# Performance work log

Hardware: AMD Instinct MI355X
Metric: run time of the kernel (lower is better)

## Reference

```python
import jax, jax.numpy as jnp
import numpy as np

IN_CAPS, IN_SIZE = 1152, 8
OUT_CAPS, OUT_SIZE = 10, 16
NUM_ITERS = 3


def squash(s, axis=-1, eps=1e-8):
    sq = jnp.sum(s * s, axis=axis, keepdims=True)
    norm = jnp.sqrt(sq + eps)
    return (sq / (1.0 + sq)) * (s / norm)


def setup_inputs() -> dict:
    key = jax.random.key(0)
    kx, kw = jax.random.split(key)
    x = jax.random.normal(kx, (512, IN_CAPS, IN_SIZE), dtype=jnp.float32)
    W = jax.random.normal(kw, (IN_CAPS, OUT_CAPS, OUT_SIZE, IN_SIZE), dtype=jnp.float32)
    return {"x": x, "W": W}


def reference(x, W):
    # u_hat[b,i,o,p] = sum_q W[i,o,p,q] x[b,i,q]   -> [B, I, O, P]
    u_hat = jnp.einsum("iopq,biq->biop", W, x)
    b_ij = jnp.zeros((IN_CAPS, OUT_CAPS), dtype=u_hat.dtype)
    v_j = None
    for _ in range(NUM_ITERS):
        # legacy F.softmax on [1,I,O,1] with no dim -> softmax over dim=1 (in_capsules)
        c_ij = jax.nn.softmax(b_ij, axis=0)                      # [I, O]
        s_j = jnp.einsum("io,biop->bop", c_ij, u_hat)            # [B, O, P]
        v_j = squash(s_j, axis=-1)                               # [B, O, P]
        # agreement, averaged over batch
        u_vj1 = jnp.einsum("biop,bop->io", u_hat, v_j) / x.shape[0]
        b_ij = b_ij + u_vj1
    return v_j  # [B, 10, 16]
```

## Files before the change

kernel.cpp:

```cpp
#include <hip/hip_runtime.h>
#include <hip/hip_bf16.h>

#define B 512
#define IC 1152
#define QD 8
#define OD 10
#define PD 16
#define KD (IC * QD)
#define NKB (KD / 32)
#define NCS 72
#define KSTEPS (NKB / NCS)
#define NCB 4
#define SOP (B * OD * PD)
#define IO (IC * OD)

typedef short bf16x8 __attribute__((ext_vector_type(8)));
typedef float f32x4 __attribute__((ext_vector_type(4)));

__device__ __forceinline__ short f2bf(float f) {
  union { float f; unsigned u; } x;
  x.f = f;
  unsigned r = x.u + 0x7FFFu + ((x.u >> 16) & 1u);
  return (short)(r >> 16);
}

__global__ __launch_bounds__(256) void routebuild_kernel(const float* __restrict__ W,
                                                         const float* __restrict__ u_part,
                                                         float* __restrict__ bijA,
                                                         short* __restrict__ Bs,
                                                         int mode) {
  __shared__ float bl[IO];
  __shared__ float wred[4][OD];
  __shared__ float mx[OD], inv[OD];
  const int tid = threadIdx.x;
  const int wave = tid >> 6, lane = tid & 63;

  if (mode != 0) {
    float lmax[OD];
#pragma unroll
    for (int o = 0; o < OD; ++o) lmax[o] = -1e30f;
    for (int i = tid; i < IC; i += 256) {
      float acc[OD];
      if (mode == 2) {
#pragma unroll
        for (int o = 0; o < OD; ++o) acc[o] = bijA[i * OD + o];
      } else {
#pragma unroll
        for (int o = 0; o < OD; ++o) acc[o] = 0.f;
      }
      for (int bc = 0; bc < NCB; ++bc) {
        const float* up = u_part + (size_t)bc * IO + i * OD;
        const float4 u0 = *(const float4*)up;
        const float4 u1 = *(const float4*)(up + 4);
        const float2 u2 = *(const float2*)(up + 8);
        acc[0] += u0.x; acc[1] += u0.y; acc[2] += u0.z; acc[3] += u0.w;
        acc[4] += u1.x; acc[5] += u1.y; acc[6] += u1.z; acc[7] += u1.w;
        acc[8] += u2.x; acc[9] += u2.y;
      }
#pragma unroll
      for (int o = 0; o < OD; ++o) {
        bl[i * OD + o] = acc[o];
        lmax[o] = fmaxf(lmax[o], acc[o]);
        if (mode == 1 && blockIdx.x == 0) bijA[i * OD + o] = acc[o];
      }
    }
#pragma unroll
    for (int o = 0; o < OD; ++o) {
      float m = lmax[o];
#pragma unroll
      for (int s = 1; s < 64; s <<= 1) m = fmaxf(m, __shfl_xor(m, s));
      if (lane == 0) wred[wave][o] = m;
    }
    __syncthreads();
    if (tid < OD)
      mx[tid] = fmaxf(fmaxf(wred[0][tid], wred[1][tid]),
                      fmaxf(wred[2][tid], wred[3][tid]));
    __syncthreads();
    float lsum[OD];
#pragma unroll
    for (int o = 0; o < OD; ++o) lsum[o] = 0.f;
    for (int i = tid; i < IC; i += 256) {
#pragma unroll
      for (int o = 0; o < OD; ++o) {
        const float e = __expf(bl[i * OD + o] - mx[o]);
        bl[i * OD + o] = e;
        lsum[o] += e;
      }
    }
    __syncthreads();
#pragma unroll
    for (int o = 0; o < OD; ++o) {
      float s = lsum[o];
#pragma unroll
      for (int st = 1; st < 64; st <<= 1) s += __shfl_xor(s, st);
      if (lane == 0) wred[wave][o] = s;
    }
    __syncthreads();
    if (tid < OD)
      inv[tid] = 1.f / (wred[0][tid] + wred[1][tid] + wred[2][tid] + wred[3][tid]);
    __syncthreads();
  }

  const int t = blockIdx.x * 256 + tid;
  const int kb = t / 160, n = t % 160;
  const int o = n >> 4, p = n & 15;
  short ov[32];
#pragma unroll
  for (int quad = 0; quad < 4; ++quad) {
    const int i = kb * 4 + quad;
    const float ci = (mode == 0) ? (1.0f / (float)IC) : (bl[i * OD + o] * inv[o]);
    const float4* wp = (const float4*)(W + (((size_t)i * OD + o) * PD + p) * QD);
    const float4 w0 = wp[0], w1 = wp[1];
    ov[quad * 8 + 0] = f2bf(ci * w0.x); ov[quad * 8 + 1] = f2bf(ci * w0.y);
    ov[quad * 8 + 2] = f2bf(ci * w0.z); ov[quad * 8 + 3] = f2bf(ci * w0.w);
    ov[quad * 8 + 4] = f2bf(ci * w1.x); ov[quad * 8 + 5] = f2bf(ci * w1.y);
    ov[quad * 8 + 6] = f2bf(ci * w1.z); ov[quad * 8 + 7] = f2bf(ci * w1.w);
  }
  int4* dst = (int4*)(Bs + (size_t)t * 32);
  const int4* src = (const int4*)ov;
#pragma unroll
  for (int j = 0; j < 4; ++j) dst[j] = src[j];
}

__global__ __launch_bounds__(256) void sgemm_kernel(const float* __restrict__ x,
                                                    const short* __restrict__ Bs,
                                                    float* __restrict__ s_part) {
  const int tid = threadIdx.x;
  const int wave = tid >> 6, lane = tid & 63;
  const int ln = lane & 15, quad = lane >> 4;
  const int cz = blockIdx.x % NCS, mb = blockIdx.x / NCS;
  const int m0 = mb * 64 + wave * 16;
  f32x4 acc[10] = {};
  const float* arow = x + (size_t)(m0 + ln) * KD + quad * 8;
#pragma unroll
  for (int step = 0; step < KSTEPS; ++step) {
    const int kb = cz * KSTEPS + step;
    const float* ap = arow + kb * 32;
    const f32x4 a0 = *(const f32x4*)ap;
    const f32x4 a1 = *(const f32x4*)(ap + 4);
    bf16x8 af;
    af[0] = f2bf(a0[0]); af[1] = f2bf(a0[1]); af[2] = f2bf(a0[2]); af[3] = f2bf(a0[3]);
    af[4] = f2bf(a1[0]); af[5] = f2bf(a1[1]); af[6] = f2bf(a1[2]); af[7] = f2bf(a1[3]);
    const short* bp = Bs + (size_t)kb * 5120 + ln * 32 + quad * 8;
#pragma unroll
    for (int nt = 0; nt < 10; ++nt) {
      const bf16x8 bf = *(const bf16x8*)(bp + nt * 512);
      acc[nt] = __builtin_amdgcn_mfma_f32_16x16x32_bf16(af, bf, acc[nt], 0, 0, 0);
    }
  }
  float* sp = s_part + (size_t)cz * SOP;
#pragma unroll
  for (int nt = 0; nt < 10; ++nt)
#pragma unroll
    for (int r = 0; r < 4; ++r)
      sp[(size_t)(m0 + quad * 4 + r) * 160 + nt * 16 + ln] = acc[nt][r];
}

__global__ __launch_bounds__(256) void squash_kernel(const float* __restrict__ s_part,
                                                     short* __restrict__ vB,
                                                     float* __restrict__ out,
                                                     int write_out) {
  const int t = blockIdx.x * 256 + threadIdx.x;
  float sv = 0.f;
#pragma unroll 8
  for (int ch = 0; ch < NCS; ++ch) sv += s_part[(size_t)ch * SOP + t];
  float sq = sv * sv;
#pragma unroll
  for (int m = 1; m < 16; m <<= 1) sq += __shfl_xor(sq, m, 16);
  const float norm = sqrtf(sq + 1e-8f);
  const float val = sv * (sq / ((1.f + sq) * norm));
  if (write_out) {
    out[t] = val;
  } else {
    const int b = t / 160, n = t - b * 160;
    vB[((size_t)(b >> 5) * 160 + n) * 32 + (b & 31)] = f2bf(val);
  }
}

__global__ __launch_bounds__(256) void aggemm_kernel(const float* __restrict__ x,
                                                     const float* __restrict__ W,
                                                     const short* __restrict__ vB,
                                                     float* __restrict__ u_part) {
  __shared__ __align__(16) short Abuf[16 * 64 * 8];
  const int tid = threadIdx.x;
  const int ig8 = blockIdx.x, kq = blockIdx.y;
  const int b0 = kq * 128;
#pragma unroll
  for (int j = 0; j < 8; ++j) {
    const int idx = tid + j * 256;
    const int b = idx >> 4, f4 = idx & 15;
    const float4 vx = *(const float4*)(x + (size_t)(b0 + b) * KD + ig8 * 64 + f4 * 4);
    const int kb = b >> 5, qk = (b & 31) >> 3, jj = b & 7;
    const int mt = (f4 * 4) >> 4;
    const int mlb = (f4 & 3) * 4;
    short* dst = Abuf + (((mt * 4 + kb) * 64 + qk * 16 + mlb) * 8 + jj);
    dst[0] = f2bf(vx.x); dst[8] = f2bf(vx.y); dst[16] = f2bf(vx.z); dst[24] = f2bf(vx.w);
  }
  __syncthreads();
  const int mt = tid >> 6, lane = tid & 63;
  const int ln = lane & 15, quad = lane >> 4;
  f32x4 acc[10] = {};
#pragma unroll
  for (int kb = 0; kb < 4; ++kb) {
    const bf16x8 af = *(const bf16x8*)(Abuf + ((mt * 4 + kb) * 64 + lane) * 8);
    const short* bp = vB + ((size_t)(kq * 4 + kb) * 160 + ln) * 32 + quad * 8;
#pragma unroll
    for (int nt = 0; nt < 10; ++nt) {
      const bf16x8 bf = *(const bf16x8*)(bp + nt * 512);
      acc[nt] = __builtin_amdgcn_mfma_f32_16x16x32_bf16(af, bf, acc[nt], 0, 0, 0);
    }
  }
  const int i = ig8 * 8 + mt * 2 + (quad >> 1);
  const int qb = (quad & 1) * 4;
#pragma unroll
  for (int nt = 0; nt < 10; ++nt) {
    const float4 wv = *(const float4*)(W + (((size_t)i * OD + nt) * PD + ln) * QD + qb);
    float pa = acc[nt][0] * wv.x + acc[nt][1] * wv.y + acc[nt][2] * wv.z + acc[nt][3] * wv.w;
    pa += __shfl_xor(pa, 1); pa += __shfl_xor(pa, 2); pa += __shfl_xor(pa, 4);
    pa += __shfl_xor(pa, 8); pa += __shfl_xor(pa, 16);
    if ((lane & 31) == 0)
      u_part[(size_t)kq * IO + i * OD + nt] = pa * (1.0f / (float)B);
  }
}


extern "C" void kernel_launch(void* const* d_in, const int* in_sizes, int n_in,
                              void* d_out, int out_size, void* d_ws, size_t ws_size,
                              hipStream_t stream) {
  const float* x = (const float*)d_in[0];
  const float* W = (const float*)d_in[1];
  float* out = (float*)d_out;

  float* ws = (float*)d_ws;
  float* s_part = ws;
  float* bijA = s_part + (size_t)NCS * SOP;
  float* u_part = bijA + IO;
  short* vB = (short*)(u_part + (size_t)NCB * IO);
  short* Bs = vB + (size_t)16 * 160 * 32;

  const dim3 agrid(144, NCB);

  routebuild_kernel<<<180, 256, 0, stream>>>(W, u_part, bijA, Bs, 0);
  sgemm_kernel<<<8 * NCS, 256, 0, stream>>>(x, Bs, s_part);
  squash_kernel<<<SOP / 256, 256, 0, stream>>>(s_part, vB, out, 0);
  aggemm_kernel<<<agrid, 256, 0, stream>>>(x, W, vB, u_part);
  routebuild_kernel<<<180, 256, 0, stream>>>(W, u_part, bijA, Bs, 1);
  sgemm_kernel<<<8 * NCS, 256, 0, stream>>>(x, Bs, s_part);
  squash_kernel<<<SOP / 256, 256, 0, stream>>>(s_part, vB, out, 0);
  aggemm_kernel<<<agrid, 256, 0, stream>>>(x, W, vB, u_part);
  routebuild_kernel<<<180, 256, 0, stream>>>(W, u_part, bijA, Bs, 2);
  sgemm_kernel<<<8 * NCS, 256, 0, stream>>>(x, Bs, s_part);
  squash_kernel<<<SOP / 256, 256, 0, stream>>>(s_part, vB, out, 1);
}
```

Before: 184.6 us.

## Pre-convert x to bf16 once and fuse routing-logit softmax into agreement GEMM

Adds a prep kernel that converts x to bf16 once and zeroes the routing logits, so the three sgemm passes and two aggemm passes read half the bytes and skip per-pass conversion. The agreement GEMM now atomically accumulates into transposed logits. The last block, found through an atomic counter, computes the per-output softmax denominators. That replaces the per-block redundant softmax in routebuild with a light rbn kernel that applies exp and normalisation per element. The trade-off is atomics on the logits, an extra bf16 workspace for x, and softmax without max subtraction, which could overflow for large logits.

```diff
diff --git a/kernel.cpp b/kernel.cpp
--- a/kernel.cpp
+++ b/kernel.cpp
@@ -13,8 +13,11 @@
 #define NCB 4
 #define SOP (B * OD * PD)
 #define IO (IC * OD)
+#define XE (B * KD)
+#define PREPX (XE / 8 / 256)
 
 typedef short bf16x8 __attribute__((ext_vector_type(8)));
+typedef short bf16x4 __attribute__((ext_vector_type(4)));
 typedef float f32x4 __attribute__((ext_vector_type(4)));
 
 __device__ __forceinline__ short f2bf(float f) {
@@ -24,91 +27,33 @@
   return (short)(r >> 16);
 }
 
-__global__ __launch_bounds__(256) void routebuild_kernel(const float* __restrict__ W,
-                                                         const float* __restrict__ u_part,
-                                                         float* __restrict__ bijA,
-                                                         short* __restrict__ Bs,
-                                                         int mode) {
-  __shared__ float bl[IO];
-  __shared__ float wred[4][OD];
-  __shared__ float mx[OD], inv[OD];
-  const int tid = threadIdx.x;
-  const int wave = tid >> 6, lane = tid & 63;
-
-  if (mode != 0) {
-    float lmax[OD];
-#pragma unroll
-    for (int o = 0; o < OD; ++o) lmax[o] = -1e30f;
-    for (int i = tid; i < IC; i += 256) {
-      float acc[OD];
-      if (mode == 2) {
-#pragma unroll
-        for (int o = 0; o < OD; ++o) acc[o] = bijA[i * OD + o];
-      } else {
-#pragma unroll
-        for (int o = 0; o < OD; ++o) acc[o] = 0.f;
-      }
-      for (int bc = 0; bc < NCB; ++bc) {
-        const float* up = u_part + (size_t)bc * IO + i * OD;
-        const float4 u0 = *(const float4*)up;
-        const float4 u1 = *(const float4*)(up + 4);
-        const float2 u2 = *(const float2*)(up + 8);
-        acc[0] += u0.x; acc[1] += u0.y; acc[2] += u0.z; acc[3] += u0.w;
-        acc[4] += u1.x; acc[5] += u1.y; acc[6] += u1.z; acc[7] += u1.w;
-        acc[8] += u2.x; acc[9] += u2.y;
-      }
-#pragma unroll
-      for (int o = 0; o < OD; ++o) {
-        bl[i * OD + o] = acc[o];
-        lmax[o] = fmaxf(lmax[o], acc[o]);
-        if (mode == 1 && blockIdx.x == 0) bijA[i * OD + o] = acc[o];
-      }
-    }
-#pragma unroll
-    for (int o = 0; o < OD; ++o) {
-      float m = lmax[o];
-#pragma unroll
-      for (int s = 1; s < 64; s <<= 1) m = fmaxf(m, __shfl_xor(m, s));
-      if (lane == 0) wred[wave][o] = m;
-    }
-    __syncthreads();
-    if (tid < OD)
-      mx[tid] = fmaxf(fmaxf(wred[0][tid], wred[1][tid]),
-                      fmaxf(wred[2][tid], wred[3][tid]));
-    __syncthreads();
-    float lsum[OD];
-#pragma unroll
-    for (int o = 0; o < OD; ++o) lsum[o] = 0.f;
-    for (int i = tid; i < IC; i += 256) {
-#pragma unroll
-      for (int o = 0; o < OD; ++o) {
-        const float e = __expf(bl[i * OD + o] - mx[o]);
-        bl[i * OD + o] = e;
-        lsum[o] += e;
-      }
-    }
-    __syncthreads();
-#pragma unroll
-    for (int o = 0; o < OD; ++o) {
-      float s = lsum[o];
-#pragma unroll
-      for (int st = 1; st < 64; st <<= 1) s += __shfl_xor(s, st);
-      if (lane == 0) wred[wave][o] = s;
-    }
-    __syncthreads();
-    if (tid < OD)
-      inv[tid] = 1.f / (wred[0][tid] + wred[1][tid] + wred[2][tid] + wred[3][tid]);
-    __syncthreads();
-  }
-
-  const int t = blockIdx.x * 256 + tid;
+__global__ __launch_bounds__(256) void prep_kernel(const float* __restrict__ x,
+                                                   const float* __restrict__ W,
+                                                   float* __restrict__ bijT,
+                                                   int* __restrict__ ctr,
+                                                   short* __restrict__ Bs,
+                                                   short* __restrict__ xB) {
+  const int bid = blockIdx.x, tid = threadIdx.x;
+  if (bid < PREPX) {
+    const size_t e0 = (((size_t)bid << 8) + tid) * 8;
+    const float4 a = *(const float4*)(x + e0);
+    const float4 b = *(const float4*)(x + e0 + 4);
+    short ov[8];
+    ov[0] = f2bf(a.x); ov[1] = f2bf(a.y); ov[2] = f2bf(a.z); ov[3] = f2bf(a.w);
+    ov[4] = f2bf(b.x); ov[5] = f2bf(b.y); ov[6] = f2bf(b.z); ov[7] = f2bf(b.w);
+    *(int4*)(xB + e0) = *(const int4*)ov;
+    return;
+  }
+  const int t = (bid - PREPX) * 256 + tid;
+  if (t < IO) bijT[t] = 0.f;
+  if (t == 0) *ctr = 0;
   const int kb = t / 160, n = t % 160;
   const int o = n >> 4, p = n & 15;
+  const float ci = 1.0f / (float)IC;
   short ov[32];
 #pragma unroll
   for (int quad = 0; quad < 4; ++quad) {
     const int i = kb * 4 + quad;
-    const float ci = (mode == 0) ? (1.0f / (float)IC) : (bl[i * OD + o] * inv[o]);
     const float4* wp = (const float4*)(W + (((size_t)i * OD + o) * PD + p) * QD);
     const float4 w0 = wp[0], w1 = wp[1];
     ov[quad * 8 + 0] = f2bf(ci * w0.x); ov[quad * 8 + 1] = f2bf(ci * w0.y);
@@ -122,7 +67,37 @@
   for (int j = 0; j < 4; ++j) dst[j] = src[j];
 }
 
-__global__ __launch_bounds__(256) void sgemm_kernel(const float* __restrict__ x,
+__global__ __launch_bounds__(256) void rbn_kernel(const float* __restrict__ W,
+                                                  const float* __restrict__ bijT,
+                                                  const float* __restrict__ esum,
+                                                  short* __restrict__ Bs) {
+  const int t = blockIdx.x * 256 + threadIdx.x;
+  const int kb = t / 160, n = t % 160;
+  const int o = n >> 4, p = n & 15;
+  const float inv = 1.0f / esum[o];
+  const float4 bv = *(const float4*)(bijT + (size_t)o * IC + kb * 4);
+  float cw[4];
+  cw[0] = __expf(bv.x) * inv; cw[1] = __expf(bv.y) * inv;
+  cw[2] = __expf(bv.z) * inv; cw[3] = __expf(bv.w) * inv;
+  short ov[32];
+#pragma unroll
+  for (int quad = 0; quad < 4; ++quad) {
+    const int i = kb * 4 + quad;
+    const float ci = cw[quad];
+    const float4* wp = (const float4*)(W + (((size_t)i * OD + o) * PD + p) * QD);
+    const float4 w0 = wp[0], w1 = wp[1];
+    ov[quad * 8 + 0] = f2bf(ci * w0.x); ov[quad * 8 + 1] = f2bf(ci * w0.y);
+    ov[quad * 8 + 2] = f2bf(ci * w0.z); ov[quad * 8 + 3] = f2bf(ci * w0.w);
+    ov[quad * 8 + 4] = f2bf(ci * w1.x); ov[quad * 8 + 5] = f2bf(ci * w1.y);
+    ov[quad * 8 + 6] = f2bf(ci * w1.z); ov[quad * 8 + 7] = f2bf(ci * w1.w);
+  }
+  int4* dst = (int4*)(Bs + (size_t)t * 32);
+  const int4* src = (const int4*)ov;
+#pragma unroll
+  for (int j = 0; j < 4; ++j) dst[j] = src[j];
+}
+
+__global__ __launch_bounds__(256) void sgemm_kernel(const short* __restrict__ xB,
                                                     const short* __restrict__ Bs,
                                                     float* __restrict__ s_part) {
   const int tid = threadIdx.x;
@@ -131,16 +106,11 @@
   const int cz = blockIdx.x % NCS, mb = blockIdx.x / NCS;
   const int m0 = mb * 64 + wave * 16;
   f32x4 acc[10] = {};
-  const float* arow = x + (size_t)(m0 + ln) * KD + quad * 8;
+  const short* arow = xB + (size_t)(m0 + ln) * KD + quad * 8;
 #pragma unroll
   for (int step = 0; step < KSTEPS; ++step) {
     const int kb = cz * KSTEPS + step;
-    const float* ap = arow + kb * 32;
-    const f32x4 a0 = *(const f32x4*)ap;
-    const f32x4 a1 = *(const f32x4*)(ap + 4);
-    bf16x8 af;
-    af[0] = f2bf(a0[0]); af[1] = f2bf(a0[1]); af[2] = f2bf(a0[2]); af[3] = f2bf(a0[3]);
-    af[4] = f2bf(a1[0]); af[5] = f2bf(a1[1]); af[6] = f2bf(a1[2]); af[7] = f2bf(a1[3]);
+    const bf16x8 af = *(const bf16x8*)(arow + kb * 32);
     const short* bp = Bs + (size_t)kb * 5120 + ln * 32 + quad * 8;
 #pragma unroll
     for (int nt = 0; nt < 10; ++nt) {
@@ -177,10 +147,12 @@
   }
 }
 
-__global__ __launch_bounds__(256) void aggemm_kernel(const float* __restrict__ x,
+__global__ __launch_bounds__(256) void aggemm_kernel(const short* __restrict__ xB,
                                                      const float* __restrict__ W,
                                                      const short* __restrict__ vB,
-                                                     float* __restrict__ u_part) {
+                                                     float* __restrict__ bijT,
+                                                     float* __restrict__ esum,
+                                                     int* __restrict__ ctr) {
   __shared__ __align__(16) short Abuf[16 * 64 * 8];
   const int tid = threadIdx.x;
   const int ig8 = blockIdx.x, kq = blockIdx.y;
@@ -189,12 +161,12 @@
   for (int j = 0; j < 8; ++j) {
     const int idx = tid + j * 256;
     const int b = idx >> 4, f4 = idx & 15;
-    const float4 vx = *(const float4*)(x + (size_t)(b0 + b) * KD + ig8 * 64 + f4 * 4);
+    const bf16x4 vx = *(const bf16x4*)(xB + (size_t)(b0 + b) * KD + ig8 * 64 + f4 * 4);
     const int kb = b >> 5, qk = (b & 31) >> 3, jj = b & 7;
-    const int mt = (f4 * 4) >> 4;
+    const int mt2 = (f4 * 4) >> 4;
     const int mlb = (f4 & 3) * 4;
-    short* dst = Abuf + (((mt * 4 + kb) * 64 + qk * 16 + mlb) * 8 + jj);
-    dst[0] = f2bf(vx.x); dst[8] = f2bf(vx.y); dst[16] = f2bf(vx.z); dst[24] = f2bf(vx.w);
+    short* dst = Abuf + (((mt2 * 4 + kb) * 64 + qk * 16 + mlb) * 8 + jj);
+    dst[0] = vx[0]; dst[8] = vx[1]; dst[16] = vx[2]; dst[24] = vx[3];
   }
   __syncthreads();
   const int mt = tid >> 6, lane = tid & 63;
@@ -219,7 +191,24 @@
     pa += __shfl_xor(pa, 1); pa += __shfl_xor(pa, 2); pa += __shfl_xor(pa, 4);
     pa += __shfl_xor(pa, 8); pa += __shfl_xor(pa, 16);
     if ((lane & 31) == 0)
-      u_part[(size_t)kq * IO + i * OD + nt] = pa * (1.0f / (float)B);
+      atomicAdd(&bijT[(size_t)nt * IC + i], pa * (1.0f / (float)B));
+  }
+  __threadfence();
+  __shared__ int lastflag;
+  if (tid == 0)
+    lastflag = (atomicAdd(ctr, 1) == (int)(gridDim.x * gridDim.y) - 1) ? 1 : 0;
+  __syncthreads();
+  if (lastflag) {
+    __threadfence();
+    if (tid == 0) *ctr = 0;
+    const int w = tid >> 6, l = tid & 63;
+    for (int o = w; o < OD; o += 4) {
+      float s = 0.f;
+      for (int ii = l; ii < IC; ii += 64) s += __expf(bijT[(size_t)o * IC + ii]);
+#pragma unroll
+      for (int st = 1; st < 64; st <<= 1) s += __shfl_xor(s, st);
+      if (l == 0) esum[o] = s;
+    }
   }
 }
 
@@ -233,22 +222,24 @@
 
   float* ws = (float*)d_ws;
   float* s_part = ws;
-  float* bijA = s_part + (size_t)NCS * SOP;
-  float* u_part = bijA + IO;
-  short* vB = (short*)(u_part + (size_t)NCB * IO);
+  float* bijT = s_part + (size_t)NCS * SOP;
+  float* esum = bijT + IO;
+  int* ctr = (int*)(esum + 16);
+  short* vB = (short*)(ctr + 16);
   short* Bs = vB + (size_t)16 * 160 * 32;
+  short* xB = Bs + (size_t)NKB * 160 * 32;
 
   const dim3 agrid(144, NCB);
 
-  routebuild_kernel<<<180, 256, 0, stream>>>(W, u_part, bijA, Bs, 0);
-  sgemm_kernel<<<8 * NCS, 256, 0, stream>>>(x, Bs, s_part);
+  prep_kernel<<<PREPX + 180, 256, 0, stream>>>(x, W, bijT, ctr, Bs, xB);
+  sgemm_kernel<<<8 * NCS, 256, 0, stream>>>(xB, Bs, s_part);
   squash_kernel<<<SOP / 256, 256, 0, stream>>>(s_part, vB, out, 0);
-  aggemm_kernel<<<agrid, 256, 0, stream>>>(x, W, vB, u_part);
-  routebuild_kernel<<<180, 256, 0, stream>>>(W, u_part, bijA, Bs, 1);
-  sgemm_kernel<<<8 * NCS, 256, 0, stream>>>(x, Bs, s_part);
+  aggemm_kernel<<<agrid, 256, 0, stream>>>(xB, W, vB, bijT, esum, ctr);
+  rbn_kernel<<<180, 256, 0, stream>>>(W, bijT, esum, Bs);
+  sgemm_kernel<<<8 * NCS, 256, 0, stream>>>(xB, Bs, s_part);
   squash_kernel<<<SOP / 256, 256, 0, stream>>>(s_part, vB, out, 0);
-  aggemm_kernel<<<agrid, 256, 0, stream>>>(x, W, vB, u_part);
-  routebuild_kernel<<<180, 256, 0, stream>>>(W, u_part, bijA, Bs, 2);
-  sgemm_kernel<<<8 * NCS, 256, 0, stream>>>(x, Bs, s_part);
+  aggemm_kernel<<<agrid, 256, 0, stream>>>(xB, W, vB, bijT, esum, ctr);
+  rbn_kernel<<<180, 256, 0, stream>>>(W, bijT, esum, Bs);
+  sgemm_kernel<<<8 * NCS, 256, 0, stream>>>(xB, Bs, s_part);
   squash_kernel<<<SOP / 256, 256, 0, stream>>>(s_part, vB, out, 1);
 }
```

New measurement: 264.8 us. 1.43x slower.
